# Optimization experiments

Hardware: AMD Instinct MI355X
Metric: run time of the kernel (lower is better)

## Reference

```python
import jax, jax.numpy as jnp
import numpy as np

B, T, I, H = 512, 128, 128, 512


def setup_inputs() -> dict:
    key = jax.random.key(0)
    ks = jax.random.split(key, 10)
    scale = 1.0 / np.sqrt(I + H)
    return {
        "s_inputs": jax.random.normal(ks[0], (B, T, I), jnp.float32),
        "l_inputs": jax.random.normal(ks[1], (B, T, I), jnp.float32),
        "dow": jax.random.randint(ks[2], (B,), 0, 7),
        "hour": jax.random.randint(ks[3], (B,), 0, 24),
        # gate weights stacked as [f, i, o, C] along output dim (math-equivalent
        # to 4 separate nn.Linear(input_size+hidden_size, hidden_size))
        "s_W": jax.random.uniform(ks[4], (I + H, 4 * H), jnp.float32, -scale, scale),
        "s_b": jax.random.uniform(ks[5], (4 * H,), jnp.float32, -scale, scale),
        "l_W": jax.random.uniform(ks[6], (I + H, 4 * H), jnp.float32, -scale, scale),
        "l_b": jax.random.uniform(ks[7], (4 * H,), jnp.float32, -scale, scale),
        "out_W": jax.random.uniform(ks[8], (2 * H, H), jnp.float32, -1.0 / np.sqrt(2 * H), 1.0 / np.sqrt(2 * H)),
        "out_b": jax.random.uniform(ks[9], (H,), jnp.float32, -1.0 / np.sqrt(2 * H), 1.0 / np.sqrt(2 * H)),
    }


def _cell(x, h, c, W, b):
    # one LSTM step: fused 4-gate GEMM then elementwise gate math
    g = jnp.concatenate([x, h], axis=1) @ W + b  # [B, 4H]
    f, i, o, cand = jnp.split(g, 4, axis=1)
    c_new = jax.nn.sigmoid(f) * c + jax.nn.sigmoid(i) * jnp.tanh(cand)
    h_new = jax.nn.sigmoid(o) * jnp.tanh(c_new)
    return h_new, c_new


def reference(s_inputs, l_inputs, dow, hour, s_W, s_b, l_W, l_b, out_W, out_b):
    batch = s_inputs.shape[0]
    hdim = out_b.shape[0]
    init = (jnp.zeros((batch, hdim), s_inputs.dtype),) * 4  # (sh, sc, lh, lc)

    def step(carry, xs):
        sh, sc, lh, lc = carry
        x_s, x_l = xs
        sh, sc = _cell(x_s, sh, sc, s_W, s_b)
        lh, lc = _cell(x_l, lh, lc, l_W, l_b)
        return (sh, sc, lh, lc), None

    xs = (jnp.swapaxes(s_inputs, 0, 1), jnp.swapaxes(l_inputs, 0, 1))  # [T,B,I]
    (sh, _, lh, _), _ = jax.lax.scan(step, init, xs)
    return jnp.tanh(jnp.concatenate([sh, lh], axis=1) @ out_W + out_b)
```

## Files before the change

kernel.cpp:

```cpp
#include <hip/hip_runtime.h>

#define HD 512
#define KD 640
#define G4 2048

typedef short short8 __attribute__((ext_vector_type(8)));
typedef __bf16 bf16x8 __attribute__((ext_vector_type(8)));
typedef float floatx4 __attribute__((ext_vector_type(4)));
typedef unsigned int uintx4 __attribute__((ext_vector_type(4)));

static __device__ __forceinline__ unsigned short f2bf(float f) {
  unsigned int u = __float_as_uint(f);
  u += 0x7fffu + ((u >> 16) & 1u);
  return (unsigned short)(u >> 16);
}
static __device__ __forceinline__ float rcp_(float x) {
  return __builtin_amdgcn_rcpf(x);
}
static __device__ __forceinline__ float sigmoidf_(float x) {
  return rcp_(1.f + __expf(-x));
}
static __device__ __forceinline__ float tanhf_(float x) {
  float ax = fabsf(x);
  float e = __expf(-2.f * ax);
  float r = fmaf(-2.f * e, rcp_(1.f + e), 1.f);
  return copysignf(r, x);
}
static __device__ __forceinline__ void store16_cc(unsigned long long a, uintx4 v) {
  asm volatile("global_store_dwordx4 %0, %1, off sc0 sc1" :: "v"(a), "v"(v) : "memory");
}
static __device__ __forceinline__ void waitcnt_vm0() {
  asm volatile("s_waitcnt vmcnt(0)" ::: "memory");
}
static __device__ __forceinline__ void load_lds16_cc(const void* g, void* l) {
  __builtin_amdgcn_global_load_lds(
      (const __attribute__((address_space(1))) void*)(unsigned long long)(uintptr_t)g,
      (__attribute__((address_space(3))) void*)l, 16, 0, 17);
}

__global__ __launch_bounds__(256) void transpose_f32_bf16(
    const float* __restrict__ src, unsigned short* __restrict__ dst,
    int R, int C) {
  __shared__ unsigned short tile[64][80];
  int nR = R >> 6;
  int tr = blockIdx.x % nR;
  int tc = blockIdx.x / nR;
  int tid = threadIdx.x;
#pragma unroll
  for (int i = 0; i < 2; ++i) {
    int seg = tid + i * 256;
    int row = seg >> 3, ks8 = (seg & 7) * 8;
    const float* p = src + (size_t)(tr * 64 + row) * C + tc * 64 + ks8;
    short8 v;
#pragma unroll
    for (int q = 0; q < 8; ++q) v[q] = (short)f2bf(p[q]);
    *(short8*)(&tile[row][ks8]) = v;
  }
  __syncthreads();
#pragma unroll
  for (int i = 0; i < 2; ++i) {
    int seg = tid + i * 256;
    int cl = seg >> 3, rs8 = (seg & 7) * 8;
    short8 v;
#pragma unroll
    for (int q = 0; q < 8; ++q) v[q] = (short)tile[rs8 + q][cl];
    *(short8*)(dst + (size_t)(tc * 64 + cl) * R + tr * 64 + rs8) = v;
  }
}

__global__ __launch_bounds__(256) void xconv(
    const float* __restrict__ xs, const float* __restrict__ xl,
    unsigned short* __restrict__ xTs, unsigned short* __restrict__ xTl) {
  int t = blockIdx.x & 127;
  int bc = (blockIdx.x >> 7) & 3;
  int which = blockIdx.x >> 9;
  const float* x = which ? xl : xs;
  unsigned short* xT = which ? xTl : xTs;
  int b0 = bc * 128;
#pragma unroll
  for (int i = 0; i < 8; ++i) {
    int seg = threadIdx.x + i * 256;
    int bl_ = seg >> 4, i8 = (seg & 15) * 8;
    const float* p = x + (size_t)(b0 + bl_) * 16384 + t * 128 + i8;
    short8 v;
#pragma unroll
    for (int q = 0; q < 8; ++q) v[q] = (short)f2bf(p[q]);
    *(short8*)(xT + ((size_t)t * 512 + b0 + bl_) * 128 + i8) = v;
  }
}

__global__ __launch_bounds__(256, 1) void lstm_persistent(
    const unsigned short* __restrict__ xTs, const unsigned short* __restrict__ xTl,
    const unsigned short* __restrict__ WTs, const unsigned short* __restrict__ WTl,
    const float* __restrict__ bs, const float* __restrict__ bl,
    unsigned short* __restrict__ hs0, unsigned short* __restrict__ hs1,
    unsigned short* __restrict__ hl0, unsigned short* __restrict__ hl1,
    int* __restrict__ flags) {
  const int bid = blockIdx.x;
  const int lstm = bid & 1;
  const int mb = (bid >> 1) & 15;
  const int nb = bid >> 5;
  const int grp = lstm * 16 + mb;
  const int b0 = mb * 32;
  const int H0 = nb * 64;

  const unsigned short* xT = lstm ? xTl : xTs;
  const unsigned short* WT = lstm ? WTl : WTs;
  const float* bias = lstm ? bl : bs;
  unsigned short* h0 = lstm ? hl0 : hs0;
  unsigned short* h1 = lstm ? hl1 : hs1;

  __shared__ unsigned short As[32][648];
  __shared__ unsigned short hbuf[32][72];

  const int tid = threadIdx.x;
  const int wn = tid >> 6;
  const int lane = tid & 63;
  const int quad = lane >> 4;
  const int lrow = lane & 15;
  const int colL = wn * 16 + lrow;

  float bias_r[4];
#pragma unroll
  for (int g = 0; g < 4; ++g) bias_r[g] = bias[g * HD + H0 + colL];
  float c_r[8];
#pragma unroll
  for (int j = 0; j < 8; ++j) c_r[j] = 0.f;

  bf16x8 breg[4][20];
#pragma unroll
  for (int g = 0; g < 4; ++g) {
    const unsigned short* wp = WT + (size_t)(g * HD + H0 + colL) * KD + quad * 8;
#pragma unroll
    for (int kc = 0; kc < 20; ++kc)
      breg[g][kc] = __builtin_bit_cast(bf16x8, *(const short8*)(wp + kc * 32));
  }

  const int st_row = tid >> 3, st_c8 = (tid & 7) * 8;
  const unsigned long long hstA =
      (unsigned long long)(h1 + (size_t)(b0 + st_row) * HD + H0 + st_c8);
  const unsigned long long hstB =
      (unsigned long long)(h0 + (size_t)(b0 + st_row) * HD + H0 + st_c8);

#pragma unroll
  for (int i = 0; i < 2; ++i) {
    int seg = tid + i * 256;
    int row = seg >> 4, ch = seg & 15;
    short8 v = *(const short8*)(xT + ((size_t)(b0 + row)) * 128 + ch * 8);
    *(short8*)(&As[row][ch * 8]) = v;
  }
#pragma unroll
  for (int i = 0; i < 8; ++i) {
    int chunk = tid + i * 256;
    int row = chunk >> 6, ch = chunk & 63;
    *(uintx4*)(&As[row][128 + ch * 8]) = (uintx4){0, 0, 0, 0};
  }

#pragma unroll 1
  for (int t = 0; t < 128; ++t) {
    const unsigned short* hr = (t & 1) ? h1 : h0;

    if (t > 0 && wn == 0) {
      while (true) {
        int v = __hip_atomic_load(flags + grp * 16 + (lane & 7),
                                  __ATOMIC_RELAXED, __HIP_MEMORY_SCOPE_AGENT);
        if (__ballot(v >= t) == 0xFFFFFFFFFFFFFFFFull) break;
        __builtin_amdgcn_s_sleep(1);
      }
    }
    __syncthreads();

    if (t > 0) {
#pragma unroll
      for (int i = 0; i < 8; ++i) {
        int row = wn + i * 4;
        load_lds16_cc(hr + (size_t)(b0 + row) * HD + lane * 8, &As[row][128]);
      }
    }

    floatx4 acc[2][4];
#pragma unroll
    for (int mt = 0; mt < 2; ++mt)
#pragma unroll
      for (int g = 0; g < 4; ++g) acc[mt][g] = (floatx4){0.f, 0.f, 0.f, 0.f};
#pragma unroll
    for (int kc = 0; kc < 4; ++kc) {
      bf16x8 a0 = __builtin_bit_cast(bf16x8, *(const short8*)(&As[lrow][kc * 32 + quad * 8]));
      bf16x8 a1 = __builtin_bit_cast(bf16x8, *(const short8*)(&As[16 + lrow][kc * 32 + quad * 8]));
#pragma unroll
      for (int g = 0; g < 4; ++g) {
        acc[0][g] = __builtin_amdgcn_mfma_f32_16x16x32_bf16(a0, breg[g][kc], acc[0][g], 0, 0, 0);
        acc[1][g] = __builtin_amdgcn_mfma_f32_16x16x32_bf16(a1, breg[g][kc], acc[1][g], 0, 0, 0);
      }
    }

    waitcnt_vm0();
    __syncthreads();

#pragma unroll
    for (int kc = 4; kc < 20; ++kc) {
      bf16x8 a0 = __builtin_bit_cast(bf16x8, *(const short8*)(&As[lrow][kc * 32 + quad * 8]));
      bf16x8 a1 = __builtin_bit_cast(bf16x8, *(const short8*)(&As[16 + lrow][kc * 32 + quad * 8]));
#pragma unroll
      for (int g = 0; g < 4; ++g) {
        acc[0][g] = __builtin_amdgcn_mfma_f32_16x16x32_bf16(a0, breg[g][kc], acc[0][g], 0, 0, 0);
        acc[1][g] = __builtin_amdgcn_mfma_f32_16x16x32_bf16(a1, breg[g][kc], acc[1][g], 0, 0, 0);
      }
    }

#pragma unroll
    for (int mt = 0; mt < 2; ++mt)
#pragma unroll
      for (int r = 0; r < 4; ++r) {
        int j = mt * 4 + r;
        float fg = acc[mt][0][r] + bias_r[0];
        float ig = acc[mt][1][r] + bias_r[1];
        float og = acc[mt][2][r] + bias_r[2];
        float cg = acc[mt][3][r] + bias_r[3];
        float cn = sigmoidf_(fg) * c_r[j] + sigmoidf_(ig) * tanhf_(cg);
        float hn = sigmoidf_(og) * tanhf_(cn);
        c_r[j] = cn;
        hbuf[mt * 16 + quad * 4 + r][colL] = f2bf(hn);
      }
    __syncthreads();

    short8 hv8 = *(const short8*)(&hbuf[st_row][st_c8]);
    store16_cc((t & 1) ? hstB : hstA, __builtin_bit_cast(uintx4, hv8));

    short8 xv[2];
    if (t < 127) {
#pragma unroll
      for (int i = 0; i < 2; ++i) {
        int seg = tid + i * 256;
        int row = seg >> 4, ch = seg & 15;
        xv[i] = *(const short8*)(xT + ((size_t)(t + 1) * 512 + b0 + row) * 128 + ch * 8);
      }
    }
    waitcnt_vm0();
    if (t < 127) {
#pragma unroll
      for (int i = 0; i < 2; ++i) {
        int seg = tid + i * 256;
        int row = seg >> 4, ch = seg & 15;
        *(short8*)(&As[row][ch * 8]) = xv[i];
      }
      if (tid == 0)
        __hip_atomic_store(flags + grp * 16 + nb, t + 1,
                           __ATOMIC_RELAXED, __HIP_MEMORY_SCOPE_AGENT);
    }
  }
}

__global__ __launch_bounds__(256) void out_gemm(
    const unsigned short* __restrict__ hs, const unsigned short* __restrict__ hl,
    const unsigned short* __restrict__ WTo,
    const float* __restrict__ ob, float* __restrict__ out) {
  const int bx = blockIdx.x;
  const int mb = bx & 7;
  const int nb = bx >> 3;

  __shared__ unsigned short As2[64][88];
  __shared__ unsigned short Bs2[128][88];

  const int tid = threadIdx.x;
  const int wave = tid >> 6;
  const int lane = tid & 63;
  const int quad = lane >> 4;
  const int lrow = lane & 15;
  const int wm = wave & 1;
  const int wn = wave >> 1;

  floatx4 acc[8];
#pragma unroll
  for (int i = 0; i < 8; ++i) acc[i] = (floatx4){0.f, 0.f, 0.f, 0.f};

  for (int k0 = 0; k0 < 1024; k0 += 64) {
#pragma unroll
    for (int i = 0; i < 2; ++i) {
      int seg = tid + i * 256;
      int row = seg >> 3, ks8 = (seg & 7) * 8;
      int kg = k0 + ks8;
      int b = mb * 64 + row;
      const unsigned short* src =
          (kg < 512) ? (hs + (size_t)b * HD + kg) : (hl + (size_t)b * HD + (kg - 512));
      *(short8*)(&As2[row][ks8]) = *(const short8*)src;
    }
#pragma unroll
    for (int i = 0; i < 4; ++i) {
      int seg = tid + i * 256;
      int n = seg >> 3, ks8 = (seg & 7) * 8;
      *(short8*)(&Bs2[n][ks8]) =
          *(const short8*)(WTo + (size_t)(nb * 128 + n) * 1024 + k0 + ks8);
    }
    __syncthreads();
#pragma unroll
    for (int ks = 0; ks < 64; ks += 32) {
      int kq = ks + quad * 8;
      bf16x8 a0 = __builtin_bit_cast(bf16x8, *(const short8*)(&As2[wm * 32 + lrow][kq]));
      bf16x8 a1 = __builtin_bit_cast(bf16x8, *(const short8*)(&As2[wm * 32 + 16 + lrow][kq]));
#pragma unroll
      for (int nt = 0; nt < 4; ++nt) {
        bf16x8 bfr = __builtin_bit_cast(bf16x8, *(const short8*)(&Bs2[wn * 64 + nt * 16 + lrow][kq]));
        acc[nt] = __builtin_amdgcn_mfma_f32_16x16x32_bf16(a0, bfr, acc[nt], 0, 0, 0);
        acc[4 + nt] = __builtin_amdgcn_mfma_f32_16x16x32_bf16(a1, bfr, acc[4 + nt], 0, 0, 0);
      }
    }
    __syncthreads();
  }
#pragma unroll
  for (int mt = 0; mt < 2; ++mt) {
#pragma unroll
    for (int nt = 0; nt < 4; ++nt) {
      int n = nb * 128 + wn * 64 + nt * 16 + lrow;
      float bv = ob[n];
#pragma unroll
      for (int r = 0; r < 4; ++r) {
        int b = mb * 64 + wm * 32 + mt * 16 + quad * 4 + r;
        out[(size_t)b * HD + n] = tanhf_(acc[mt * 4 + nt][r] + bv);
      }
    }
  }
}

extern "C" void kernel_launch(void* const* d_in, const int* in_sizes, int n_in,
                              void* d_out, int out_size, void* d_ws, size_t ws_size,
                              hipStream_t stream) {
  (void)in_sizes; (void)n_in; (void)out_size; (void)ws_size;
  const float* xs = (const float*)d_in[0];
  const float* xl = (const float*)d_in[1];
  const float* sW = (const float*)d_in[4];
  const float* sb = (const float*)d_in[5];
  const float* lW = (const float*)d_in[6];
  const float* lb = (const float*)d_in[7];
  const float* oW = (const float*)d_in[8];
  const float* ob = (const float*)d_in[9];

  char* w = (char*)d_ws;
  int* flags = (int*)w;
  unsigned short* WTs = (unsigned short*)(w + 4096);
  unsigned short* WTl = WTs + (size_t)G4 * KD;
  unsigned short* WTo = WTl + (size_t)G4 * KD;
  unsigned short* xTs = WTo + (size_t)HD * 1024;
  unsigned short* xTl = xTs + (size_t)128 * 512 * 128;
  unsigned short* hs0 = xTl + (size_t)128 * 512 * 128;
  unsigned short* hs1 = hs0 + (size_t)512 * HD;
  unsigned short* hl0 = hs1 + (size_t)512 * HD;
  unsigned short* hl1 = hl0 + (size_t)512 * HD;

  hipMemsetAsync(flags, 0, 4096, stream);
  transpose_f32_bf16<<<(640 / 64) * (2048 / 64), 256, 0, stream>>>(sW, WTs, 640, 2048);
  transpose_f32_bf16<<<(640 / 64) * (2048 / 64), 256, 0, stream>>>(lW, WTl, 640, 2048);
  transpose_f32_bf16<<<(1024 / 64) * (512 / 64), 256, 0, stream>>>(oW, WTo, 1024, 512);
  xconv<<<1024, 256, 0, stream>>>(xs, xl, xTs, xTl);

  const float* sbp = sb; const float* lbp = lb;
  const unsigned short *xTs_c = xTs, *xTl_c = xTl, *WTs_c = WTs, *WTl_c = WTl;
  unsigned short *a_hs0 = hs0, *a_hs1 = hs1, *a_hl0 = hl0, *a_hl1 = hl1;
  int* a_flags = flags;
  void* args[] = {(void*)&xTs_c, (void*)&xTl_c, (void*)&WTs_c, (void*)&WTl_c,
                  (void*)&sbp, (void*)&lbp, (void*)&a_hs0, (void*)&a_hs1,
                  (void*)&a_hl0, (void*)&a_hl1, (void*)&a_flags};
  hipError_t e = hipLaunchCooperativeKernel((const void*)lstm_persistent,
                                            dim3(256), dim3(256), args, 0, stream);
  if (e != hipSuccess) {
    lstm_persistent<<<256, 256, 0, stream>>>(xTs, xTl, WTs, WTl, sb, lb,
                                             hs0, hs1, hl0, hl1, flags);
  }
  out_gemm<<<32, 256, 0, stream>>>(hs0, hl0, WTo, ob, (float*)d_out);
}
```

Before: 741.5 us.

## Fuse prep kernels, convert x inline, and split h-wait per row half

Merges the three weight transposes and the flag memset into one prep launch, and drops the separate x conversion pass so each timestep's fp32 input is converted to bf16 directly into LDS inside the persistent kernel. The h-dependent part of the GEMM is split so the first 16-row half starts after a partial vmcnt wait, overlapping the second half's LDS loads. Readiness flags become per-wave instead of per-block, which removes a block barrier before the flag store. This cuts launch count and the x round-trip through memory, at the cost of fp32 global loads and conversion on the recurrent critical path. The t=0 step now skips the h part entirely instead of multiplying against a zeroed buffer.

New measurement: 936.9 us. 26.3% more time.

```diff
diff --git a/kernel.cpp b/kernel.cpp
--- a/kernel.cpp
+++ b/kernel.cpp
@@ -32,20 +32,36 @@
 static __device__ __forceinline__ void waitcnt_vm0() {
   asm volatile("s_waitcnt vmcnt(0)" ::: "memory");
 }
+static __device__ __forceinline__ void waitcnt_vm4() {
+  asm volatile("s_waitcnt vmcnt(4)" ::: "memory");
+}
+static __device__ __forceinline__ void raw_barrier() {
+  asm volatile("s_barrier" ::: "memory");
+}
 static __device__ __forceinline__ void load_lds16_cc(const void* g, void* l) {
   __builtin_amdgcn_global_load_lds(
       (const __attribute__((address_space(1))) void*)(unsigned long long)(uintptr_t)g,
       (__attribute__((address_space(3))) void*)l, 16, 0, 17);
 }
 
-__global__ __launch_bounds__(256) void transpose_f32_bf16(
-    const float* __restrict__ src, unsigned short* __restrict__ dst,
-    int R, int C) {
+__global__ __launch_bounds__(256) void prep(
+    const float* __restrict__ sW, const float* __restrict__ lW,
+    const float* __restrict__ oW,
+    unsigned short* __restrict__ WTs, unsigned short* __restrict__ WTl,
+    unsigned short* __restrict__ WTo, int* __restrict__ flags) {
+  const int bx = blockIdx.x;
+  const int tid = threadIdx.x;
+  if (bx >= 768) {
+    for (int i = tid; i < 1024; i += 256) flags[i] = 0;
+    return;
+  }
   __shared__ unsigned short tile[64][80];
+  const float* src; unsigned short* dst; int R, C, idx;
+  if (bx < 320)      { src = sW; dst = WTs; R = 640;  C = 2048; idx = bx; }
+  else if (bx < 640) { src = lW; dst = WTl; R = 640;  C = 2048; idx = bx - 320; }
+  else               { src = oW; dst = WTo; R = 1024; C = 512;  idx = bx - 640; }
   int nR = R >> 6;
-  int tr = blockIdx.x % nR;
-  int tc = blockIdx.x / nR;
-  int tid = threadIdx.x;
+  int tr = idx % nR, tc = idx / nR;
 #pragma unroll
   for (int i = 0; i < 2; ++i) {
     int seg = tid + i * 256;
@@ -68,29 +84,8 @@
   }
 }
 
-__global__ __launch_bounds__(256) void xconv(
+__global__ __launch_bounds__(256, 1) void lstm_persistent(
     const float* __restrict__ xs, const float* __restrict__ xl,
-    unsigned short* __restrict__ xTs, unsigned short* __restrict__ xTl) {
-  int t = blockIdx.x & 127;
-  int bc = (blockIdx.x >> 7) & 3;
-  int which = blockIdx.x >> 9;
-  const float* x = which ? xl : xs;
-  unsigned short* xT = which ? xTl : xTs;
-  int b0 = bc * 128;
-#pragma unroll
-  for (int i = 0; i < 8; ++i) {
-    int seg = threadIdx.x + i * 256;
-    int bl_ = seg >> 4, i8 = (seg & 15) * 8;
-    const float* p = x + (size_t)(b0 + bl_) * 16384 + t * 128 + i8;
-    short8 v;
-#pragma unroll
-    for (int q = 0; q < 8; ++q) v[q] = (short)f2bf(p[q]);
-    *(short8*)(xT + ((size_t)t * 512 + b0 + bl_) * 128 + i8) = v;
-  }
-}
-
-__global__ __launch_bounds__(256, 1) void lstm_persistent(
-    const unsigned short* __restrict__ xTs, const unsigned short* __restrict__ xTl,
     const unsigned short* __restrict__ WTs, const unsigned short* __restrict__ WTl,
     const float* __restrict__ bs, const float* __restrict__ bl,
     unsigned short* __restrict__ hs0, unsigned short* __restrict__ hs1,
@@ -104,7 +99,7 @@
   const int b0 = mb * 32;
   const int H0 = nb * 64;
 
-  const unsigned short* xT = lstm ? xTl : xTs;
+  const float* x = lstm ? xl : xs;
   const unsigned short* WT = lstm ? WTl : WTs;
   const float* bias = lstm ? bl : bs;
   unsigned short* h0 = lstm ? hl0 : hs0;
@@ -142,27 +137,29 @@
   const unsigned long long hstB =
       (unsigned long long)(h0 + (size_t)(b0 + st_row) * HD + H0 + st_c8);
 
-#pragma unroll
-  for (int i = 0; i < 2; ++i) {
-    int seg = tid + i * 256;
-    int row = seg >> 4, ch = seg & 15;
-    short8 v = *(const short8*)(xT + ((size_t)(b0 + row)) * 128 + ch * 8);
-    *(short8*)(&As[row][ch * 8]) = v;
-  }
-#pragma unroll
-  for (int i = 0; i < 8; ++i) {
-    int chunk = tid + i * 256;
-    int row = chunk >> 6, ch = chunk & 63;
-    *(uintx4*)(&As[row][128 + ch * 8]) = (uintx4){0, 0, 0, 0};
-  }
+  auto stage_x = [&](int tt) {
+#pragma unroll
+    for (int i = 0; i < 2; ++i) {
+      int seg = tid + i * 256;
+      int row = seg >> 4, ch = seg & 15;
+      const float* p = x + (size_t)(b0 + row) * 16384 + tt * 128 + ch * 8;
+      short8 v;
+#pragma unroll
+      for (int q = 0; q < 8; ++q) v[q] = (short)f2bf(p[q]);
+      *(short8*)(&As[row][ch * 8]) = v;
+    }
+  };
+
+  stage_x(0);
 
 #pragma unroll 1
   for (int t = 0; t < 128; ++t) {
     const unsigned short* hr = (t & 1) ? h1 : h0;
 
     if (t > 0 && wn == 0) {
+      const int fidx = grp * 32 + (lane & 31);
       while (true) {
-        int v = __hip_atomic_load(flags + grp * 16 + (lane & 7),
+        int v = __hip_atomic_load(flags + fidx,
                                   __ATOMIC_RELAXED, __HIP_MEMORY_SCOPE_AGENT);
         if (__ballot(v >= t) == 0xFFFFFFFFFFFFFFFFull) break;
         __builtin_amdgcn_s_sleep(1);
@@ -194,17 +191,24 @@
       }
     }
 
-    waitcnt_vm0();
-    __syncthreads();
-
-#pragma unroll
-    for (int kc = 4; kc < 20; ++kc) {
-      bf16x8 a0 = __builtin_bit_cast(bf16x8, *(const short8*)(&As[lrow][kc * 32 + quad * 8]));
-      bf16x8 a1 = __builtin_bit_cast(bf16x8, *(const short8*)(&As[16 + lrow][kc * 32 + quad * 8]));
-#pragma unroll
-      for (int g = 0; g < 4; ++g) {
-        acc[0][g] = __builtin_amdgcn_mfma_f32_16x16x32_bf16(a0, breg[g][kc], acc[0][g], 0, 0, 0);
-        acc[1][g] = __builtin_amdgcn_mfma_f32_16x16x32_bf16(a1, breg[g][kc], acc[1][g], 0, 0, 0);
+    if (t > 0) {
+      waitcnt_vm4();
+      raw_barrier();
+#pragma unroll
+      for (int kc = 4; kc < 20; ++kc) {
+        bf16x8 a0 = __builtin_bit_cast(bf16x8, *(const short8*)(&As[lrow][kc * 32 + quad * 8]));
+#pragma unroll
+        for (int g = 0; g < 4; ++g)
+          acc[0][g] = __builtin_amdgcn_mfma_f32_16x16x32_bf16(a0, breg[g][kc], acc[0][g], 0, 0, 0);
+      }
+      waitcnt_vm0();
+      raw_barrier();
+#pragma unroll
+      for (int kc = 4; kc < 20; ++kc) {
+        bf16x8 a1 = __builtin_bit_cast(bf16x8, *(const short8*)(&As[16 + lrow][kc * 32 + quad * 8]));
+#pragma unroll
+        for (int g = 0; g < 4; ++g)
+          acc[1][g] = __builtin_amdgcn_mfma_f32_16x16x32_bf16(a1, breg[g][kc], acc[1][g], 0, 0, 0);
       }
     }
 
@@ -226,28 +230,11 @@
 
     short8 hv8 = *(const short8*)(&hbuf[st_row][st_c8]);
     store16_cc((t & 1) ? hstB : hstA, __builtin_bit_cast(uintx4, hv8));
-
-    short8 xv[2];
-    if (t < 127) {
-#pragma unroll
-      for (int i = 0; i < 2; ++i) {
-        int seg = tid + i * 256;
-        int row = seg >> 4, ch = seg & 15;
-        xv[i] = *(const short8*)(xT + ((size_t)(t + 1) * 512 + b0 + row) * 128 + ch * 8);
-      }
-    }
     waitcnt_vm0();
-    if (t < 127) {
-#pragma unroll
-      for (int i = 0; i < 2; ++i) {
-        int seg = tid + i * 256;
-        int row = seg >> 4, ch = seg & 15;
-        *(short8*)(&As[row][ch * 8]) = xv[i];
-      }
-      if (tid == 0)
-        __hip_atomic_store(flags + grp * 16 + nb, t + 1,
-                           __ATOMIC_RELAXED, __HIP_MEMORY_SCOPE_AGENT);
-    }
+    if (lane == 0 && t < 127)
+      __hip_atomic_store(flags + grp * 32 + nb * 4 + wn, t + 1,
+                         __ATOMIC_RELAXED, __HIP_MEMORY_SCOPE_AGENT);
+    if (t < 127) stage_x(t + 1);
   }
 }
 
@@ -340,30 +327,25 @@
   unsigned short* WTs = (unsigned short*)(w + 4096);
   unsigned short* WTl = WTs + (size_t)G4 * KD;
   unsigned short* WTo = WTl + (size_t)G4 * KD;
-  unsigned short* xTs = WTo + (size_t)HD * 1024;
-  unsigned short* xTl = xTs + (size_t)128 * 512 * 128;
-  unsigned short* hs0 = xTl + (size_t)128 * 512 * 128;
+  unsigned short* hs0 = WTo + (size_t)HD * 1024;
   unsigned short* hs1 = hs0 + (size_t)512 * HD;
   unsigned short* hl0 = hs1 + (size_t)512 * HD;
   unsigned short* hl1 = hl0 + (size_t)512 * HD;
 
-  hipMemsetAsync(flags, 0, 4096, stream);
-  transpose_f32_bf16<<<(640 / 64) * (2048 / 64), 256, 0, stream>>>(sW, WTs, 640, 2048);
-  transpose_f32_bf16<<<(640 / 64) * (2048 / 64), 256, 0, stream>>>(lW, WTl, 640, 2048);
-  transpose_f32_bf16<<<(1024 / 64) * (512 / 64), 256, 0, stream>>>(oW, WTo, 1024, 512);
-  xconv<<<1024, 256, 0, stream>>>(xs, xl, xTs, xTl);
-
+  prep<<<769, 256, 0, stream>>>(sW, lW, oW, WTs, WTl, WTo, flags);
+
+  const float* xsp = xs; const float* xlp = xl;
   const float* sbp = sb; const float* lbp = lb;
-  const unsigned short *xTs_c = xTs, *xTl_c = xTl, *WTs_c = WTs, *WTl_c = WTl;
+  const unsigned short *WTs_c = WTs, *WTl_c = WTl;
   unsigned short *a_hs0 = hs0, *a_hs1 = hs1, *a_hl0 = hl0, *a_hl1 = hl1;
   int* a_flags = flags;
-  void* args[] = {(void*)&xTs_c, (void*)&xTl_c, (void*)&WTs_c, (void*)&WTl_c,
+  void* args[] = {(void*)&xsp, (void*)&xlp, (void*)&WTs_c, (void*)&WTl_c,
                   (void*)&sbp, (void*)&lbp, (void*)&a_hs0, (void*)&a_hs1,
                   (void*)&a_hl0, (void*)&a_hl1, (void*)&a_flags};
   hipError_t e = hipLaunchCooperativeKernel((const void*)lstm_persistent,
                                             dim3(256), dim3(256), args, 0, stream);
   if (e != hipSuccess) {
-    lstm_persistent<<<256, 256, 0, stream>>>(xTs, xTl, WTs, WTl, sb, lb,
+    lstm_persistent<<<256, 256, 0, stream>>>(xs, xl, WTs, WTl, sb, lb,
                                              hs0, hs1, hl0, hl1, flags);
   }
   out_gemm<<<32, 256, 0, stream>>>(hs0, hl0, WTo, ob, (float*)d_out);
```
